# Optimization experiments

Hardware: AMD Instinct MI355X
Metric: run time of the kernel (lower is better)

Reference implementation:

```python
import jax, jax.numpy as jnp
import numpy as np

ALPHA = 0.2  # LeakyReLU negative slope
N, F_IN, F_OUT = 8192, 512, 64
NEG_INF = -9e15


def setup_inputs() -> dict:
    key = jax.random.key(0)
    k1, k2, k3, k4 = jax.random.split(key, 4)
    inp = jax.random.normal(k1, (N, F_IN), dtype=jnp.float32)
    adj = jax.random.randint(k2, (N, N), 0, 2, dtype=jnp.int32)
    W = jax.random.normal(k3, (F_IN, F_OUT), dtype=jnp.float32) * (1.414 / np.sqrt(F_IN))
    a = jax.random.normal(k4, (2 * F_OUT, 1), dtype=jnp.float32) * 0.1
    return {"input": inp, "adj": adj, "W": W, "a": a, "sparse": 0}


def reference(input, adj, W, a, sparse):
    h = input @ W  # [N, F_out]
    # Decompose concat([h_i, h_j]) @ a into additive src/dst terms (same math,
    # avoids the O(N^2 * 2F) intermediate): e_ij = leakyrelu(h_i@a1 + h_j@a2)
    f_src = h @ a[:F_OUT]   # [N, 1]
    f_dst = h @ a[F_OUT:]   # [N, 1]
    e = jax.nn.leaky_relu(f_src + f_dst.T, ALPHA)  # [N, N]
    attention = jnp.where(adj > 0, e, NEG_INF)
    attention = jax.nn.softmax(attention, axis=1)
    h_prime = attention @ h  # [N, F_out]
    return jax.nn.leaky_relu(h_prime, 0.01)[None]  # concat=True path; default F.leaky_relu slope 0.01
```

## Files before the change

### kernel.cpp

```cpp
#include <hip/hip_runtime.h>
#include <hip/hip_bf16.h>

#define N 8192
#define FIN 512
#define FOUT 64
#define ALPHA 0.2f

typedef __bf16 bf16x8 __attribute__((ext_vector_type(8)));
typedef float f32x4 __attribute__((ext_vector_type(4)));
typedef int i32x4 __attribute__((ext_vector_type(4)));


__device__ __forceinline__ unsigned enc_f(float x) {
    unsigned u = __float_as_uint(x);
    return (u & 0x80000000u) ? ~u : (u | 0x80000000u);
}
__device__ __forceinline__ float dec_f(unsigned u) {
    return (u & 0x80000000u) ? __uint_as_float(u & 0x7FFFFFFFu) : __uint_as_float(~u);
}

__global__ __launch_bounds__(64) void k_wt(const float* __restrict__ W,
                                           __bf16* __restrict__ WtG) {
    const int g = blockIdx.x * 64 + threadIdx.x;
    const int k = g >> 3;
    const int f0 = (g & 7) * 8;
    const float4 w0 = *(const float4*)(W + (size_t)k * FOUT + f0);
    const float4 w1 = *(const float4*)(W + (size_t)k * FOUT + f0 + 4);
    WtG[(size_t)(f0 + 0) * FIN + k] = (__bf16)w0.x;
    WtG[(size_t)(f0 + 1) * FIN + k] = (__bf16)w0.y;
    WtG[(size_t)(f0 + 2) * FIN + k] = (__bf16)w0.z;
    WtG[(size_t)(f0 + 3) * FIN + k] = (__bf16)w0.w;
    WtG[(size_t)(f0 + 4) * FIN + k] = (__bf16)w1.x;
    WtG[(size_t)(f0 + 5) * FIN + k] = (__bf16)w1.y;
    WtG[(size_t)(f0 + 6) * FIN + k] = (__bf16)w1.z;
    WtG[(size_t)(f0 + 7) * FIN + k] = (__bf16)w1.w;
}

__global__ __launch_bounds__(64) void k12(const float* __restrict__ in,
                                          const __bf16* __restrict__ WtG,
                                          const float* __restrict__ a,
                                          float* __restrict__ f_src,
                                          float* __restrict__ f_dst,
                                          unsigned* __restrict__ Mkey,
                                          __bf16* __restrict__ hT) {
    __shared__ __bf16 tb[64][16];
    const int lane = threadIdx.x;
    const int m = lane & 15, quad = lane >> 4;
    const int i0 = blockIdx.x * 16;

    f32x4 acc[4];
#pragma unroll
    for (int t = 0; t < 4; ++t) acc[t] = (f32x4){0.f, 0.f, 0.f, 0.f};

    const float* arow = in + (size_t)(i0 + m) * FIN + quad * 8;
    for (int k0 = 0; k0 < FIN; k0 += 32) {
        const float4 x0 = *(const float4*)(arow + k0);
        const float4 x1 = *(const float4*)(arow + k0 + 4);
        bf16x8 af;
        af[0] = (__bf16)x0.x; af[1] = (__bf16)x0.y; af[2] = (__bf16)x0.z; af[3] = (__bf16)x0.w;
        af[4] = (__bf16)x1.x; af[5] = (__bf16)x1.y; af[6] = (__bf16)x1.z; af[7] = (__bf16)x1.w;
#pragma unroll
        for (int t = 0; t < 4; ++t) {
            const bf16x8 bf = *(const bf16x8*)(WtG + (size_t)(t * 16 + m) * FIN + k0 + quad * 8);
            acc[t] = __builtin_amdgcn_mfma_f32_16x16x32_bf16(af, bf, acc[t], 0, 0, 0);
        }
    }
    float s1[4], s2[4];
#pragma unroll
    for (int r = 0; r < 4; ++r) { s1[r] = 0.f; s2[r] = 0.f; }
#pragma unroll
    for (int t = 0; t < 4; ++t) {
        const float a1 = a[t * 16 + m], a2 = a[64 + t * 16 + m];
#pragma unroll
        for (int r = 0; r < 4; ++r) {
            s1[r] += acc[t][r] * a1;
            s2[r] += acc[t][r] * a2;
        }
    }
#pragma unroll
    for (int off = 1; off <= 8; off <<= 1)
#pragma unroll
        for (int r = 0; r < 4; ++r) {
            s1[r] += __shfl_xor(s1[r], off);
            s2[r] += __shfl_xor(s2[r], off);
        }
    float lm = -1e30f;
    if (m == 0) {
#pragma unroll
        for (int r = 0; r < 4; ++r) {
            f_src[i0 + quad * 4 + r] = s1[r];
            f_dst[i0 + quad * 4 + r] = s2[r];
            lm = fmaxf(lm, s2[r]);
        }
    }
    lm = fmaxf(lm, __shfl_xor(lm, 16));
    lm = fmaxf(lm, __shfl_xor(lm, 32));
    if (lane == 0) atomicMax(Mkey, enc_f(lm));

#pragma unroll
    for (int t = 0; t < 4; ++t)
#pragma unroll
        for (int r = 0; r < 4; ++r) tb[t * 16 + m][quad * 4 + r] = (__bf16)acc[t][r];
    __syncthreads();
    {
        const int f = lane;
        const bf16x8 v0 = *(const bf16x8*)&tb[f][0];
        const bf16x8 v1 = *(const bf16x8*)&tb[f][8];
        *(bf16x8*)(hT + (size_t)f * N + i0) = v0;
        *(bf16x8*)(hT + (size_t)f * N + i0 + 8) = v1;
    }
}

constexpr int JT = 256;

__global__ __launch_bounds__(256, 4) void k3_attn(const int* __restrict__ adj,
                                                  const float* __restrict__ f_src,
                                                  const float* __restrict__ fdstG,
                                                  const unsigned* __restrict__ Mkey,
                                                  const __bf16* __restrict__ hT,
                                                  float* __restrict__ num,
                                                  float* __restrict__ lsum) {
    __shared__ __bf16 sh[64][JT + 8];
    __shared__ float sfd[JT];
    const int tid = threadIdx.x;
    const int wv = tid >> 6, lane = tid & 63;
    const int m = lane & 15, quad = lane >> 4;
    const int i0 = blockIdx.x * 64 + wv * 16;
    const int jbase = blockIdx.y * 1024;
    const float LOG2E = 1.44269504088896f;

    const float M = dec_f(*Mkey);
    const float fs = f_src[i0 + m];
    const float t0 = fs + M;
    const float shift = fmaxf(t0, ALPHA * t0);

    f32x4 acc[4];
#pragma unroll
    for (int t = 0; t < 4; ++t) acc[t] = (f32x4){0.f, 0.f, 0.f, 0.f};
    f32x4 accl = (f32x4){0.f, 0.f, 0.f, 0.f};

    bf16x8 bones;
#pragma unroll
    for (int jj = 0; jj < 8; ++jj) bones[jj] = (__bf16)(m == 0 ? 1.0f : 0.0f);

    const int* arow = adj + (size_t)(i0 + m) * N;

    for (int jt = jbase; jt < jbase + 1024; jt += JT) {
        __syncthreads();
#pragma unroll
        for (int c = tid; c < 64 * JT / 8; c += 256) {
            const int f = c >> 5, off = (c & 31) * 8;
            *(bf16x8*)&sh[f][off] = *(const bf16x8*)(hT + (size_t)f * N + jt + off);
        }
        if (tid < 64) *(f32x4*)&sfd[tid * 4] = *(const f32x4*)(fdstG + jt + tid * 4);
        __syncthreads();

#pragma unroll
        for (int jj0 = 0; jj0 < JT; jj0 += 64) {
            const int* p = arow + jt + jj0 + quad * 8;
            i32x4 A[4];
            A[0] = __builtin_nontemporal_load((const i32x4*)p);
            A[1] = __builtin_nontemporal_load((const i32x4*)(p + 4));
            A[2] = __builtin_nontemporal_load((const i32x4*)(p + 32));
            A[3] = __builtin_nontemporal_load((const i32x4*)(p + 36));
            const f32x4 D0 = *(const f32x4*)&sfd[jj0 + quad * 8];
            const f32x4 D1 = *(const f32x4*)&sfd[jj0 + quad * 8 + 4];
            const f32x4 D2 = *(const f32x4*)&sfd[jj0 + 32 + quad * 8];
            const f32x4 D3 = *(const f32x4*)&sfd[jj0 + 32 + quad * 8 + 4];
#pragma unroll
            for (int u = 0; u < 2; ++u) {
                const i32x4 Aa = A[u * 2], Ab = A[u * 2 + 1];
                const f32x4 Da = u ? D2 : D0, Db = u ? D3 : D1;
                float wvv[8];
#pragma unroll
                for (int jj = 0; jj < 8; ++jj) {
                    const float fd = jj < 4 ? Da[jj] : Db[jj - 4];
                    const int am = jj < 4 ? Aa[jj] : Ab[jj - 4];
                    float e = fs + fd;
                    e = fmaxf(e, ALPHA * e);
                    const float ex = __builtin_amdgcn_exp2f((e - shift) * LOG2E);
                    wvv[jj] = am > 0 ? ex : 0.f;
                }
                bf16x8 af;
#pragma unroll
                for (int jj = 0; jj < 8; ++jj) af[jj] = (__bf16)wvv[jj];
#pragma unroll
                for (int t = 0; t < 4; ++t) {
                    const bf16x8 bfr =
                        *(const bf16x8*)&sh[t * 16 + m][jj0 + u * 32 + quad * 8];
                    acc[t] = __builtin_amdgcn_mfma_f32_16x16x32_bf16(af, bfr, acc[t], 0, 0, 0);
                }
                accl = __builtin_amdgcn_mfma_f32_16x16x32_bf16(af, bones, accl, 0, 0, 0);
            }
        }
    }
#pragma unroll
    for (int t = 0; t < 4; ++t)
#pragma unroll
        for (int r = 0; r < 4; ++r)
            atomicAdd(&num[(size_t)(i0 + quad * 4 + r) * FOUT + t * 16 + m], acc[t][r]);
    if (m == 0) {
#pragma unroll
        for (int r = 0; r < 4; ++r) atomicAdd(&lsum[i0 + quad * 4 + r], accl[r]);
    }
}

__global__ __launch_bounds__(256) void k4_norm(float* __restrict__ out,
                                               const float* __restrict__ lsum) {
    const int idx = blockIdx.x * 256 + threadIdx.x;
    const float l = lsum[idx >> 6];
    const float v = out[idx] / (l > 0.f ? l : 1.f);
    out[idx] = v > 0.f ? v : 0.01f * v;
}

extern "C" void kernel_launch(void* const* d_in, const int* in_sizes, int n_in,
                              void* d_out, int out_size, void* d_ws, size_t ws_size,
                              hipStream_t stream) {
    const float* in = (const float*)d_in[0];
    const int* adj = (const int*)d_in[1];
    const float* W = (const float*)d_in[2];
    const float* a = (const float*)d_in[3];
    float* out = (float*)d_out;

    char* ws = (char*)d_ws;
    unsigned* Mkey = (unsigned*)ws;
    float* lsum = (float*)(ws + 64);
    float* f_src = (float*)(ws + 32832);
    float* f_dst = (float*)(ws + 65600);
    __bf16* WtG = (__bf16*)(ws + 98368);
    __bf16* hT = (__bf16*)(ws + 163904);

    hipMemsetAsync(ws, 0, 64 + N * 4, stream);
    hipMemsetAsync(d_out, 0, (size_t)N * FOUT * sizeof(float), stream);

    k_wt<<<64, 64, 0, stream>>>(W, WtG);
    k12<<<N / 16, 64, 0, stream>>>(in, WtG, a, f_src, f_dst, Mkey, hT);

    dim3 g3(N / 64, 8);
    k3_attn<<<g3, 256, 0, stream>>>(adj, f_src, f_dst, Mkey, hT, out, lsum);
    k4_norm<<<(N * FOUT) / 256, 256, 0, stream>>>(out, lsum);
}
```

Baseline: 418.8 us.

## Drop LDS staging in attention kernel and prefetch adjacency one step ahead

```diff
diff --git a/kernel.cpp b/kernel.cpp
--- a/kernel.cpp
+++ b/kernel.cpp
@@ -111,22 +111,18 @@
     }
 }
 
-constexpr int JT = 256;
-
-__global__ __launch_bounds__(256, 4) void k3_attn(const int* __restrict__ adj,
-                                                  const float* __restrict__ f_src,
-                                                  const float* __restrict__ fdstG,
-                                                  const unsigned* __restrict__ Mkey,
-                                                  const __bf16* __restrict__ hT,
-                                                  float* __restrict__ num,
-                                                  float* __restrict__ lsum) {
-    __shared__ __bf16 sh[64][JT + 8];
-    __shared__ float sfd[JT];
+__global__ __launch_bounds__(256) void k3_attn(const int* __restrict__ adj,
+                                               const float* __restrict__ f_src,
+                                               const float* __restrict__ fdstG,
+                                               const unsigned* __restrict__ Mkey,
+                                               const __bf16* __restrict__ hT,
+                                               float* __restrict__ num,
+                                               float* __restrict__ lsum) {
     const int tid = threadIdx.x;
     const int wv = tid >> 6, lane = tid & 63;
     const int m = lane & 15, quad = lane >> 4;
-    const int i0 = blockIdx.x * 64 + wv * 16;
-    const int jbase = blockIdx.y * 1024;
+    const int i0 = (blockIdx.x * 4 + wv) * 16;
+    const int jc = blockIdx.y * 1024;
     const float LOG2E = 1.44269504088896f;
 
     const float M = dec_f(*Mkey);
@@ -145,55 +141,60 @@
 
     const int* arow = adj + (size_t)(i0 + m) * N;
 
-    for (int jt = jbase; jt < jbase + 1024; jt += JT) {
-        __syncthreads();
-#pragma unroll
-        for (int c = tid; c < 64 * JT / 8; c += 256) {
-            const int f = c >> 5, off = (c & 31) * 8;
-            *(bf16x8*)&sh[f][off] = *(const bf16x8*)(hT + (size_t)f * N + jt + off);
-        }
-        if (tid < 64) *(f32x4*)&sfd[tid * 4] = *(const f32x4*)(fdstG + jt + tid * 4);
-        __syncthreads();
-
-#pragma unroll
-        for (int jj0 = 0; jj0 < JT; jj0 += 64) {
-            const int* p = arow + jt + jj0 + quad * 8;
-            i32x4 A[4];
-            A[0] = __builtin_nontemporal_load((const i32x4*)p);
-            A[1] = __builtin_nontemporal_load((const i32x4*)(p + 4));
-            A[2] = __builtin_nontemporal_load((const i32x4*)(p + 32));
-            A[3] = __builtin_nontemporal_load((const i32x4*)(p + 36));
-            const f32x4 D0 = *(const f32x4*)&sfd[jj0 + quad * 8];
-            const f32x4 D1 = *(const f32x4*)&sfd[jj0 + quad * 8 + 4];
-            const f32x4 D2 = *(const f32x4*)&sfd[jj0 + 32 + quad * 8];
-            const f32x4 D3 = *(const f32x4*)&sfd[jj0 + 32 + quad * 8 + 4];
-#pragma unroll
-            for (int u = 0; u < 2; ++u) {
-                const i32x4 Aa = A[u * 2], Ab = A[u * 2 + 1];
-                const f32x4 Da = u ? D2 : D0, Db = u ? D3 : D1;
-                float wvv[8];
-#pragma unroll
-                for (int jj = 0; jj < 8; ++jj) {
-                    const float fd = jj < 4 ? Da[jj] : Db[jj - 4];
-                    const int am = jj < 4 ? Aa[jj] : Ab[jj - 4];
-                    float e = fs + fd;
-                    e = fmaxf(e, ALPHA * e);
-                    const float ex = __builtin_amdgcn_exp2f((e - shift) * LOG2E);
-                    wvv[jj] = am > 0 ? ex : 0.f;
-                }
-                bf16x8 af;
-#pragma unroll
-                for (int jj = 0; jj < 8; ++jj) af[jj] = (__bf16)wvv[jj];
-#pragma unroll
-                for (int t = 0; t < 4; ++t) {
-                    const bf16x8 bfr =
-                        *(const bf16x8*)&sh[t * 16 + m][jj0 + u * 32 + quad * 8];
-                    acc[t] = __builtin_amdgcn_mfma_f32_16x16x32_bf16(af, bfr, acc[t], 0, 0, 0);
-                }
-                accl = __builtin_amdgcn_mfma_f32_16x16x32_bf16(af, bones, accl, 0, 0, 0);
+    i32x4 A[4];
+    f32x4 D[4];
+#define LOADJ(Adst, Ddst, J0)                                                   \
+    {                                                                           \
+        const int* p = arow + (J0) + quad * 8;                                  \
+        Adst[0] = __builtin_nontemporal_load((const i32x4*)p);                  \
+        Adst[1] = __builtin_nontemporal_load((const i32x4*)(p + 4));            \
+        Adst[2] = __builtin_nontemporal_load((const i32x4*)(p + 32));           \
+        Adst[3] = __builtin_nontemporal_load((const i32x4*)(p + 36));           \
+        const float* q = fdstG + (J0) + quad * 8;                               \
+        Ddst[0] = *(const f32x4*)q;                                             \
+        Ddst[1] = *(const f32x4*)(q + 4);                                       \
+        Ddst[2] = *(const f32x4*)(q + 32);                                      \
+        Ddst[3] = *(const f32x4*)(q + 36);                                      \
+    }
+
+    LOADJ(A, D, jc)
+
+    for (int j0 = jc; j0 < jc + 1024; j0 += 64) {
+        const int jn = (j0 + 64 < jc + 1024) ? j0 + 64 : j0;
+        i32x4 Bn[4];
+        f32x4 En[4];
+        LOADJ(Bn, En, jn)
+
+#pragma unroll
+        for (int u = 0; u < 2; ++u) {
+            const i32x4 Aa = A[u * 2], Ab = A[u * 2 + 1];
+            const f32x4 Da = D[u * 2], Db = D[u * 2 + 1];
+            float wvv[8];
+#pragma unroll
+            for (int jj = 0; jj < 8; ++jj) {
+                const float fd = jj < 4 ? Da[jj] : Db[jj - 4];
+                const int am = jj < 4 ? Aa[jj] : Ab[jj - 4];
+                float e = fs + fd;
+                e = fmaxf(e, ALPHA * e);
+                const float ex = __builtin_amdgcn_exp2f((e - shift) * LOG2E);
+                wvv[jj] = am > 0 ? ex : 0.f;
             }
-        }
-    }
+            bf16x8 af;
+#pragma unroll
+            for (int jj = 0; jj < 8; ++jj) af[jj] = (__bf16)wvv[jj];
+#pragma unroll
+            for (int t = 0; t < 4; ++t) {
+                const bf16x8 bfr =
+                    *(const bf16x8*)(hT + (size_t)(t * 16 + m) * N + j0 + u * 32 + quad * 8);
+                acc[t] = __builtin_amdgcn_mfma_f32_16x16x32_bf16(af, bfr, acc[t], 0, 0, 0);
+            }
+            accl = __builtin_amdgcn_mfma_f32_16x16x32_bf16(af, bones, accl, 0, 0, 0);
+        }
+#pragma unroll
+        for (int x = 0; x < 4; ++x) { A[x] = Bn[x]; D[x] = En[x]; }
+    }
+#undef LOADJ
+
 #pragma unroll
     for (int t = 0; t < 4; ++t)
 #pragma unroll
```

Measured after the change: 454.8 us. 1.09x slower.

## Split attention into 512-column chunks with partial buffers and register prefetch of adj

Applied to the files above, without the earlier changes.

```diff
diff --git a/kernel.cpp b/kernel.cpp
--- a/kernel.cpp
+++ b/kernel.cpp
@@ -9,6 +9,10 @@
 typedef __bf16 bf16x8 __attribute__((ext_vector_type(8)));
 typedef float f32x4 __attribute__((ext_vector_type(4)));
 typedef int i32x4 __attribute__((ext_vector_type(4)));
+
+constexpr int JC = 512;
+constexpr int NCH = N / JC;
+constexpr int STR = JC + 8;
 
 
 __device__ __forceinline__ unsigned enc_f(float x) {
@@ -111,23 +115,29 @@
     }
 }
 
-constexpr int JT = 256;
-
-__global__ __launch_bounds__(256, 4) void k3_attn(const int* __restrict__ adj,
-                                                  const float* __restrict__ f_src,
-                                                  const float* __restrict__ fdstG,
-                                                  const unsigned* __restrict__ Mkey,
-                                                  const __bf16* __restrict__ hT,
-                                                  float* __restrict__ num,
-                                                  float* __restrict__ lsum) {
-    __shared__ __bf16 sh[64][JT + 8];
-    __shared__ float sfd[JT];
+__global__ __launch_bounds__(256) void k3_attn(const int* __restrict__ adj,
+                                               const float* __restrict__ f_src,
+                                               const float* __restrict__ fdstG,
+                                               const unsigned* __restrict__ Mkey,
+                                               const __bf16* __restrict__ hT,
+                                               float* __restrict__ pnum,
+                                               float* __restrict__ plsum) {
+    __shared__ __bf16 sh[64 * STR];
+    __shared__ float sfd[JC];
     const int tid = threadIdx.x;
     const int wv = tid >> 6, lane = tid & 63;
     const int m = lane & 15, quad = lane >> 4;
-    const int i0 = blockIdx.x * 64 + wv * 16;
-    const int jbase = blockIdx.y * 1024;
+    const int i0 = (blockIdx.x * 4 + wv) * 16;
+    const int jc = blockIdx.y * JC;
     const float LOG2E = 1.44269504088896f;
+
+#pragma unroll
+    for (int c = tid; c < 64 * JC / 8; c += 256) {
+        const int f = c >> 6, off = (c & 63) * 8;
+        *(bf16x8*)&sh[f * STR + off] = *(const bf16x8*)(hT + (size_t)f * N + jc + off);
+    }
+    if (tid < JC / 4) *(f32x4*)&sfd[tid * 4] = *(const f32x4*)(fdstG + jc + tid * 4);
+    __syncthreads();
 
     const float M = dec_f(*Mkey);
     const float fs = f_src[i0 + m];
@@ -143,73 +153,84 @@
 #pragma unroll
     for (int jj = 0; jj < 8; ++jj) bones[jj] = (__bf16)(m == 0 ? 1.0f : 0.0f);
 
-    const int* arow = adj + (size_t)(i0 + m) * N;
-
-    for (int jt = jbase; jt < jbase + 1024; jt += JT) {
-        __syncthreads();
-#pragma unroll
-        for (int c = tid; c < 64 * JT / 8; c += 256) {
-            const int f = c >> 5, off = (c & 31) * 8;
-            *(bf16x8*)&sh[f][off] = *(const bf16x8*)(hT + (size_t)f * N + jt + off);
-        }
-        if (tid < 64) *(f32x4*)&sfd[tid * 4] = *(const f32x4*)(fdstG + jt + tid * 4);
-        __syncthreads();
-
-#pragma unroll
-        for (int jj0 = 0; jj0 < JT; jj0 += 64) {
-            const int* p = arow + jt + jj0 + quad * 8;
-            i32x4 A[4];
-            A[0] = __builtin_nontemporal_load((const i32x4*)p);
-            A[1] = __builtin_nontemporal_load((const i32x4*)(p + 4));
-            A[2] = __builtin_nontemporal_load((const i32x4*)(p + 32));
-            A[3] = __builtin_nontemporal_load((const i32x4*)(p + 36));
-            const f32x4 D0 = *(const f32x4*)&sfd[jj0 + quad * 8];
-            const f32x4 D1 = *(const f32x4*)&sfd[jj0 + quad * 8 + 4];
-            const f32x4 D2 = *(const f32x4*)&sfd[jj0 + 32 + quad * 8];
-            const f32x4 D3 = *(const f32x4*)&sfd[jj0 + 32 + quad * 8 + 4];
-#pragma unroll
-            for (int u = 0; u < 2; ++u) {
-                const i32x4 Aa = A[u * 2], Ab = A[u * 2 + 1];
-                const f32x4 Da = u ? D2 : D0, Db = u ? D3 : D1;
-                float wvv[8];
-#pragma unroll
-                for (int jj = 0; jj < 8; ++jj) {
-                    const float fd = jj < 4 ? Da[jj] : Db[jj - 4];
-                    const int am = jj < 4 ? Aa[jj] : Ab[jj - 4];
-                    float e = fs + fd;
-                    e = fmaxf(e, ALPHA * e);
-                    const float ex = __builtin_amdgcn_exp2f((e - shift) * LOG2E);
-                    wvv[jj] = am > 0 ? ex : 0.f;
-                }
-                bf16x8 af;
-#pragma unroll
-                for (int jj = 0; jj < 8; ++jj) af[jj] = (__bf16)wvv[jj];
-#pragma unroll
-                for (int t = 0; t < 4; ++t) {
-                    const bf16x8 bfr =
-                        *(const bf16x8*)&sh[t * 16 + m][jj0 + u * 32 + quad * 8];
-                    acc[t] = __builtin_amdgcn_mfma_f32_16x16x32_bf16(af, bfr, acc[t], 0, 0, 0);
-                }
-                accl = __builtin_amdgcn_mfma_f32_16x16x32_bf16(af, bones, accl, 0, 0, 0);
+    const int* arow = adj + (size_t)(i0 + m) * N + jc;
+
+    i32x4 buf[3][4];
+#pragma unroll
+    for (int p = 0; p < 3; ++p) {
+        const int* q = arow + p * 64 + quad * 8;
+        buf[p][0] = __builtin_nontemporal_load((const i32x4*)q);
+        buf[p][1] = __builtin_nontemporal_load((const i32x4*)(q + 4));
+        buf[p][2] = __builtin_nontemporal_load((const i32x4*)(q + 32));
+        buf[p][3] = __builtin_nontemporal_load((const i32x4*)(q + 36));
+    }
+
+#pragma unroll
+    for (int it = 0; it < 8; ++it) {
+        i32x4 cur[4];
+#pragma unroll
+        for (int x = 0; x < 4; ++x) cur[x] = buf[it % 3][x];
+        if (it + 3 < 8) {
+            const int* q = arow + (it + 3) * 64 + quad * 8;
+            buf[it % 3][0] = __builtin_nontemporal_load((const i32x4*)q);
+            buf[it % 3][1] = __builtin_nontemporal_load((const i32x4*)(q + 4));
+            buf[it % 3][2] = __builtin_nontemporal_load((const i32x4*)(q + 32));
+            buf[it % 3][3] = __builtin_nontemporal_load((const i32x4*)(q + 36));
+        }
+        const int jloc = it * 64;
+#pragma unroll
+        for (int u = 0; u < 2; ++u) {
+            const i32x4 Aa = cur[u * 2], Ab = cur[u * 2 + 1];
+            const f32x4 Da = *(const f32x4*)&sfd[jloc + u * 32 + quad * 8];
+            const f32x4 Db = *(const f32x4*)&sfd[jloc + u * 32 + quad * 8 + 4];
+            float wvv[8];
+#pragma unroll
+            for (int jj = 0; jj < 8; ++jj) {
+                const float fd = jj < 4 ? Da[jj] : Db[jj - 4];
+                const int am = jj < 4 ? Aa[jj] : Ab[jj - 4];
+                float e = fs + fd;
+                e = fmaxf(e, ALPHA * e);
+                const float ex = __builtin_amdgcn_exp2f((e - shift) * LOG2E);
+                wvv[jj] = am > 0 ? ex : 0.f;
             }
-        }
-    }
+            bf16x8 af;
+#pragma unroll
+            for (int jj = 0; jj < 8; ++jj) af[jj] = (__bf16)wvv[jj];
+#pragma unroll
+            for (int t = 0; t < 4; ++t) {
+                const bf16x8 bfr =
+                    *(const bf16x8*)&sh[(t * 16 + m) * STR + jloc + u * 32 + quad * 8];
+                acc[t] = __builtin_amdgcn_mfma_f32_16x16x32_bf16(af, bfr, acc[t], 0, 0, 0);
+            }
+            accl = __builtin_amdgcn_mfma_f32_16x16x32_bf16(af, bones, accl, 0, 0, 0);
+        }
+    }
+
+    float* pn = pnum + (size_t)blockIdx.y * N * FOUT;
 #pragma unroll
     for (int t = 0; t < 4; ++t)
 #pragma unroll
         for (int r = 0; r < 4; ++r)
-            atomicAdd(&num[(size_t)(i0 + quad * 4 + r) * FOUT + t * 16 + m], acc[t][r]);
+            pn[(size_t)(i0 + quad * 4 + r) * FOUT + t * 16 + m] = acc[t][r];
     if (m == 0) {
 #pragma unroll
-        for (int r = 0; r < 4; ++r) atomicAdd(&lsum[i0 + quad * 4 + r], accl[r]);
-    }
-}
-
-__global__ __launch_bounds__(256) void k4_norm(float* __restrict__ out,
-                                               const float* __restrict__ lsum) {
+        for (int r = 0; r < 4; ++r)
+            plsum[(size_t)blockIdx.y * N + i0 + quad * 4 + r] = accl[r];
+    }
+}
+
+__global__ __launch_bounds__(256) void k4_norm(const float* __restrict__ pnum,
+                                               const float* __restrict__ plsum,
+                                               float* __restrict__ out) {
     const int idx = blockIdx.x * 256 + threadIdx.x;
-    const float l = lsum[idx >> 6];
-    const float v = out[idx] / (l > 0.f ? l : 1.f);
+    const int row = idx >> 6;
+    float s = 0.f, l = 0.f;
+#pragma unroll
+    for (int c = 0; c < NCH; ++c) {
+        s += pnum[(size_t)c * N * FOUT + idx];
+        l += plsum[(size_t)c * N + row];
+    }
+    const float v = s / (l > 0.f ? l : 1.f);
     out[idx] = v > 0.f ? v : 0.01f * v;
 }
 
@@ -224,19 +245,19 @@
 
     char* ws = (char*)d_ws;
     unsigned* Mkey = (unsigned*)ws;
-    float* lsum = (float*)(ws + 64);
-    float* f_src = (float*)(ws + 32832);
-    float* f_dst = (float*)(ws + 65600);
-    __bf16* WtG = (__bf16*)(ws + 98368);
-    __bf16* hT = (__bf16*)(ws + 163904);
-
-    hipMemsetAsync(ws, 0, 64 + N * 4, stream);
-    hipMemsetAsync(d_out, 0, (size_t)N * FOUT * sizeof(float), stream);
+    float* f_src = (float*)(ws + 4096);
+    float* f_dst = (float*)(ws + 36864);
+    __bf16* WtG = (__bf16*)(ws + 69632);
+    __bf16* hT = (__bf16*)(ws + 135168);
+    float* plsum = (float*)(ws + 2097152);
+    float* pnum = (float*)(ws + 4194304);
+
+    hipMemsetAsync(ws, 0, 64, stream);
 
     k_wt<<<64, 64, 0, stream>>>(W, WtG);
     k12<<<N / 16, 64, 0, stream>>>(in, WtG, a, f_src, f_dst, Mkey, hT);
 
-    dim3 g3(N / 64, 8);
-    k3_attn<<<g3, 256, 0, stream>>>(adj, f_src, f_dst, Mkey, hT, out, lsum);
-    k4_norm<<<(N * FOUT) / 256, 256, 0, stream>>>(out, lsum);
-}
+    dim3 g3(N / 64, NCH);
+    k3_attn<<<g3, 256, 0, stream>>>(adj, f_src, f_dst, Mkey, hT, pnum, plsum);
+    k4_norm<<<(N * FOUT) / 256, 256, 0, stream>>>(pnum, plsum, out);
+}
```

Measured after the change: 428.0 us. +2.2%, slower.
